# Kernel optimization log

Measured on AMD Instinct MI355X. Metric: run time of the kernel, lower is better.

Reference implementation:

```python
import jax, jax.numpy as jnp
import numpy as np

NUM_TOKENS = 16384
HIDDEN = 4096
NUM_EXPERTS = 256
TOP_K = 8
N_GROUP = 8
TOPK_GROUP = 4
NORM_TOPK_PROB = True
ROUTED_SCALING_FACTOR = 1.0


def setup_inputs() -> dict:
    key = jax.random.key(0)
    k1, k2, k3 = jax.random.split(key, 3)
    hidden_states = jax.random.normal(k1, (NUM_TOKENS, HIDDEN), dtype=jnp.float32)
    weight = jax.random.normal(k2, (NUM_EXPERTS, HIDDEN), dtype=jnp.float32) * (HIDDEN ** -0.5)
    e_score_correction_bias = jax.random.normal(k3, (NUM_EXPERTS,), dtype=jnp.float32) * 0.01
    return {"hidden_states": hidden_states, "weight": weight,
            "e_score_correction_bias": e_score_correction_bias}


def reference(hidden_states, weight, e_score_correction_bias):
    num_tokens = hidden_states.shape[0]
    # router logits: [T, E]
    logits = jnp.einsum('th,eh->te', hidden_states.astype(jnp.float32),
                        weight.astype(jnp.float32))
    scores = jax.nn.sigmoid(logits)
    scores_for_choice = scores + e_score_correction_bias[None, :]
    # group scores: sum of top-2 within each group, [T, G]
    per_group = scores_for_choice.reshape(num_tokens, N_GROUP, NUM_EXPERTS // N_GROUP)
    top2_vals, _ = jax.lax.top_k(per_group, 2)
    group_scores = top2_vals.sum(axis=-1)
    # select topk_group groups, build mask over experts
    _, group_idx = jax.lax.top_k(group_scores, TOPK_GROUP)  # [T, topk_group]
    group_mask = jnp.zeros_like(group_scores).at[
        jnp.arange(num_tokens)[:, None], group_idx].set(1.0)  # [T, G]
    score_mask = jnp.repeat(group_mask, NUM_EXPERTS // N_GROUP, axis=1)  # [T, E]
    tmp_scores = jnp.where(score_mask > 0, scores_for_choice, -jnp.inf)
    # final top-k experts over masked scores
    _, topk_idx = jax.lax.top_k(tmp_scores, TOP_K)  # [T, K]
    topk_weight = jnp.take_along_axis(scores, topk_idx, axis=1)
    if TOP_K > 1 and NORM_TOPK_PROB:
        denom = topk_weight.sum(axis=-1, keepdims=True) + 1e-20
        topk_weight = topk_weight / denom
    topk_weight = topk_weight * ROUTED_SCALING_FACTOR
    return logits, topk_weight, topk_idx
```

## Files before the change

kernel.cpp:

```cpp
#include <hip/hip_runtime.h>
#include <hip/hip_bf16.h>
#include <math.h>

#define TKN 16384
#define HID 4096
#define NE  256
#define TOPK 8
#define NGRP 8
#define TOPG 4

#define BM 64
#define BK 64
#define NKT (HID / BK)
#define BIMG 16384

typedef _Float16 half8 __attribute__((ext_vector_type(8)));
typedef float    f32x4 __attribute__((ext_vector_type(4)));

static __device__ __forceinline__ unsigned pkrtz(float x, float y) {
    auto r = __builtin_amdgcn_cvt_pkrtz(x, y);
    return __builtin_bit_cast(unsigned, r);
}
static __device__ __forceinline__ float hi_mask(float a) {
    return __uint_as_float(__float_as_uint(a) & 0xFFFFE000u);
}
static __device__ __forceinline__ void split_w(const float4 v,
    unsigned char* hiP, unsigned char* loP, int ofs)
{
    const float h0 = hi_mask(v.x), h1 = hi_mask(v.y),
                h2 = hi_mask(v.z), h3 = hi_mask(v.w);
    *(uint2*)(hiP + ofs) = make_uint2(pkrtz(h0, h1), pkrtz(h2, h3));
    *(uint2*)(loP + ofs) = make_uint2(pkrtz(v.x - h0, v.y - h1),
                                      pkrtz(v.z - h2, v.w - h3));
}

__global__ __launch_bounds__(256) void prep_b(const float* __restrict__ B,
                                              unsigned char* __restrict__ ws)
{
    const int gid = blockIdx.x * 256 + threadIdx.x;
    const int e   = gid >> 9;
    const int k0  = (gid & 511) * 8;
    const float* src = B + (size_t)e * HID + k0;
    float v[8];
    #pragma unroll
    for (int i = 0; i < 8; ++i) v[i] = src[i];
    unsigned hw[4], lw[4];
    #pragma unroll
    for (int j = 0; j < 4; ++j) {
        const float x0 = v[2*j], x1 = v[2*j+1];
        const float h0 = hi_mask(x0), h1 = hi_mask(x1);
        hw[j] = pkrtz(h0, h1);
        lw[j] = pkrtz(x0 - h0, x1 - h1);
    }
    const int cb     = e >> 6;
    const int colgrp = (e & 63) >> 4;
    const int lane16 = e & 15;
    const int kt     = k0 >> 6;
    const int kk     = k0 & 63;
    const int wg     = kk >> 5;
    const int kseg   = (kk >> 3) & 3;
    const int f      = colgrp * 2 + wg;
    unsigned char* img = ws + (size_t)(cb * NKT + kt) * BIMG
                            + f * 2048 + (kseg * 16 + lane16) * 16;
    *(uint4*)(img)        = make_uint4(hw[0], hw[1], hw[2], hw[3]);
    *(uint4*)(img + 1024) = make_uint4(lw[0], lw[1], lw[2], lw[3]);
}

__global__ __launch_bounds__(256, 3) void gemm_mfma(
    const float* __restrict__ A, const unsigned char* __restrict__ Bws,
    float* __restrict__ C)
{
    __shared__ __align__(16) unsigned char smem[2][2][8192];

    const int tid  = threadIdx.x;
    const int lane = tid & 63;
    const int wave = tid >> 6;
    const int wg = wave >> 1;
    const int wc = wave & 1;

    const int logical = (blockIdx.x & 7) * 128 + (blockIdx.x >> 3);
    const int mb   = logical >> 2;
    const int cb   = logical & 3;
    const int row0 = mb * BM;

    const float* srcp[4];
    int wofs[4];
    #pragma unroll
    for (int i = 0; i < 4; ++i) {
        const int r = i * 16 + wave * 4 + (lane >> 4);
        srcp[i] = A + (size_t)(row0 + r) * HID + (lane & 15) * 4;
        wofs[i] = r * 128 + (((lane & 15) * 8) ^ ((r & 7) << 4));
    }

    const int kx    = ((wg * 64) + ((lane >> 4) << 4)) ^ ((lane & 7) << 4);
    const int aRowB = (lane & 15) * 128;

    const unsigned char* bBase = Bws + (size_t)cb * NKT * BIMG;
    const int f0off = ((wc * 2 + 0) * 2 + wg) * 2048 + lane * 16;
    const int f1off = ((wc * 2 + 1) * 2 + wg) * 2048 + lane * 16;

    f32x4 acc[4][2];
    #pragma unroll
    for (int i = 0; i < 4; ++i) { acc[i][0] = (f32x4)0.f; acc[i][1] = (f32x4)0.f; }

    float4 aA[4], aB[4];
    half8  bA[4], bB[4];

    {
        float4 p[4];
        #pragma unroll
        for (int i = 0; i < 4; ++i) p[i] = *(const float4*)(srcp[i]);
        #pragma unroll
        for (int i = 0; i < 4; ++i)
            split_w(p[i], &smem[0][0][0], &smem[0][1][0], wofs[i]);
    }
    #pragma unroll
    for (int i = 0; i < 4; ++i) aB[i] = *(const float4*)(srcp[i] + BK);
    bA[0] = *(const half8*)(bBase + f0off);
    bA[1] = *(const half8*)(bBase + f0off + 1024);
    bA[2] = *(const half8*)(bBase + f1off);
    bA[3] = *(const half8*)(bBase + f1off + 1024);
    __syncthreads();

#define PSTEP(T, RBUF, WBUF, ASPL, AISS, BCUR, BNXT)                           \
    {                                                                          \
        const int t_ = (T);                                                    \
        if (t_ + 2 < NKT) {               \
            _Pragma("unroll")                                                  \
            for (int i = 0; i < 4; ++i)                                        \
                AISS[i] = *(const float4*)(srcp[i] + (t_ + 2) * BK);           \
        }                                                                      \
        if (t_ + 1 < NKT) {               \
            const unsigned char* bp = bBase + (size_t)(t_ + 1) * BIMG;         \
            BNXT[0] = *(const half8*)(bp + f0off);                             \
            BNXT[1] = *(const half8*)(bp + f0off + 1024);                      \
            BNXT[2] = *(const half8*)(bp + f1off);                             \
            BNXT[3] = *(const half8*)(bp + f1off + 1024);                      \
        }                                                                      \
                     \
        asm volatile("s_waitcnt lgkmcnt(0)\n\ts_barrier" ::: "memory");        \
        if (t_ + 1 < NKT) {         \
            _Pragma("unroll")                                                  \
            for (int i = 0; i < 4; ++i)                                        \
                split_w(ASPL[i], &WBUF[0][0], &WBUF[1][0], wofs[i]);           \
        }                                                                      \
        _Pragma("unroll")                                                      \
        for (int mt = 0; mt < 4; ++mt) {                                       \
            const half8 ah = *(const half8*)(&RBUF[0][0] + aRowB + mt * 2048 + kx); \
            const half8 al = *(const half8*)(&RBUF[1][0] + aRowB + mt * 2048 + kx); \
            f32x4 c0 = acc[mt][0];                                             \
            c0 = __builtin_amdgcn_mfma_f32_16x16x32_f16(ah, BCUR[0], c0, 0, 0, 0); \
            c0 = __builtin_amdgcn_mfma_f32_16x16x32_f16(ah, BCUR[1], c0, 0, 0, 0); \
            c0 = __builtin_amdgcn_mfma_f32_16x16x32_f16(al, BCUR[0], c0, 0, 0, 0); \
            acc[mt][0] = c0;                                                   \
            f32x4 c1 = acc[mt][1];                                             \
            c1 = __builtin_amdgcn_mfma_f32_16x16x32_f16(ah, BCUR[2], c1, 0, 0, 0); \
            c1 = __builtin_amdgcn_mfma_f32_16x16x32_f16(ah, BCUR[3], c1, 0, 0, 0); \
            c1 = __builtin_amdgcn_mfma_f32_16x16x32_f16(al, BCUR[3 - 1], c1, 0, 0, 0); \
            acc[mt][1] = c1;                                                   \
        }                                                                      \
    }

    for (int kt = 0; kt < NKT; kt += 2) {
        PSTEP(kt,     smem[0], smem[1], aB, aA, bA, bB);
        PSTEP(kt + 1, smem[1], smem[0], aA, aB, bB, bA);
    }
#undef PSTEP

    float* redf = (float*)&smem[0][0][0];
    const int fb = wc * 2048 + lane * 4;
    if (wg == 1) {
        #pragma unroll
        for (int mt = 0; mt < 4; ++mt)
            #pragma unroll
            for (int nt = 0; nt < 2; ++nt)
                *(f32x4*)&redf[fb + (mt * 2 + nt) * 256] = acc[mt][nt];
    }
    __syncthreads();
    if (wg == 0) {
        #pragma unroll
        for (int mt = 0; mt < 4; ++mt) {
            #pragma unroll
            for (int nt = 0; nt < 2; ++nt) {
                f32x4 o = acc[mt][nt] + *(const f32x4*)&redf[fb + (mt * 2 + nt) * 256];
                const int r0 = row0 + mt * 16 + (lane >> 4) * 4;
                const int cc = cb * 64 + wc * 32 + nt * 16 + (lane & 15);
                #pragma unroll
                for (int r = 0; r < 4; ++r)
                    C[(size_t)(r0 + r) * NE + cc] = o[r];
            }
        }
    }
}

__global__ __launch_bounds__(256) void router_topk_kernel(
    const float* __restrict__ logits, const float* __restrict__ bias,
    float* __restrict__ out_w, float* __restrict__ out_i)
{
    const int wid  = threadIdx.x >> 6;
    const int lane = threadIdx.x & 63;
    const int token = blockIdx.x * 4 + wid;

    const float* row = logits + (size_t)token * NE;
    const float4 lg = *(const float4*)&row[lane * 4];

    float sig[4], sc[4];
    {
        const float l4[4] = {lg.x, lg.y, lg.z, lg.w};
        #pragma unroll
        for (int j = 0; j < 4; ++j) {
            sig[j] = 1.f / (1.f + expf(-l4[j]));
            sc[j]  = sig[j] + bias[lane * 4 + j];
        }
    }

    float m1 = sc[0], m2 = -INFINITY;
    #pragma unroll
    for (int j = 1; j < 4; ++j) {
        if (sc[j] > m1) { m2 = m1; m1 = sc[j]; }
        else if (sc[j] > m2) { m2 = sc[j]; }
    }
    #pragma unroll
    for (int off = 1; off < 8; off <<= 1) {
        const float o1 = __shfl_xor(m1, off);
        const float o2 = __shfl_xor(m2, off);
        const float lo = fminf(m1, o1);
        m1 = fmaxf(m1, o1);
        m2 = fmaxf(lo, fmaxf(m2, o2));
    }
    const float gscore = m1 + m2;

    const int gmy = lane >> 3;
    int rank = 0;
    #pragma unroll
    for (int g = 0; g < NGRP; ++g) {
        const float gs = __shfl(gscore, g * 8);
        if (gs > gscore || (gs == gscore && g < gmy)) ++rank;
    }
    if (rank >= TOPG) {
        #pragma unroll
        for (int j = 0; j < 4; ++j) sc[j] = -INFINITY;
    }

    float wk[TOPK]; int ik[TOPK];
    float wsum = 0.f;
    #pragma unroll
    for (int k = 0; k < TOPK; ++k) {
        float bv = sc[0]; int bi = lane * 4;
        #pragma unroll
        for (int j = 1; j < 4; ++j)
            if (sc[j] > bv) { bv = sc[j]; bi = lane * 4 + j; }
        #pragma unroll
        for (int off = 1; off < 64; off <<= 1) {
            const float v2 = __shfl_xor(bv, off);
            const int   i2 = __shfl_xor(bi, off);
            if (v2 > bv || (v2 == bv && i2 < bi)) { bv = v2; bi = i2; }
        }
        const int owner = bi >> 2;
        const int j = bi & 3;
        const float sv = (j == 0) ? sig[0] : (j == 1) ? sig[1] : (j == 2) ? sig[2] : sig[3];
        const float w = __shfl(sv, owner);
        wk[k] = w; ik[k] = bi; wsum += w;
        if (lane == owner) {
            if (j == 0) sc[0] = -INFINITY;
            else if (j == 1) sc[1] = -INFINITY;
            else if (j == 2) sc[2] = -INFINITY;
            else sc[3] = -INFINITY;
        }
    }

    if (lane == 0) {
        const float denom = wsum + 1e-20f;
        #pragma unroll
        for (int k = 0; k < TOPK; ++k) {
            out_w[(size_t)token * TOPK + k] = wk[k] / denom;
            out_i[(size_t)token * TOPK + k] = (float)ik[k];
        }
    }
}

extern "C" void kernel_launch(void* const* d_in, const int* in_sizes, int n_in,
                              void* d_out, int out_size, void* d_ws, size_t ws_size,
                              hipStream_t stream) {
    const float* hidden = (const float*)d_in[0];
    const float* weight = (const float*)d_in[1];
    const float* bias   = (const float*)d_in[2];

    float* logits = (float*)d_out;
    float* out_w  = logits + (size_t)TKN * NE;
    float* out_i  = out_w + (size_t)TKN * TOPK;

    unsigned char* bpl = (unsigned char*)d_ws;

    prep_b<<<512, 256, 0, stream>>>(weight, bpl);
    gemm_mfma<<<1024, 256, 0, stream>>>(hidden, bpl, logits);
    router_topk_kernel<<<TKN / 4, 256, 0, stream>>>(logits, bias, out_w, out_i);
}
```

Measured before the change: 169.9 us.

## Deepen A-tile register prefetch to three stages and hoist LDS fragment reads

Rotates four register buffers for the fp32 A tile so global loads are issued three k-steps ahead instead of two. The loop is unrolled by four, with sched_barriers pinning load issue order. All A fragments for the current tile are read from LDS before the split-and-write of the next tile, so the LDS reads overlap the conversion work and the MFMAs see ready operands. This costs more VGPRs, which may lower occupancy.

```diff
diff --git a/kernel.cpp b/kernel.cpp
--- a/kernel.cpp
+++ b/kernel.cpp
@@ -103,67 +103,81 @@
     #pragma unroll
     for (int i = 0; i < 4; ++i) { acc[i][0] = (f32x4)0.f; acc[i][1] = (f32x4)0.f; }
 
-    float4 aA[4], aB[4];
+    float4 a0[4], a1[4], a2[4], a3[4];
     half8  bA[4], bB[4];
 
-    {
-        float4 p[4];
-        #pragma unroll
-        for (int i = 0; i < 4; ++i) p[i] = *(const float4*)(srcp[i]);
-        #pragma unroll
-        for (int i = 0; i < 4; ++i)
-            split_w(p[i], &smem[0][0][0], &smem[0][1][0], wofs[i]);
-    }
-    #pragma unroll
-    for (int i = 0; i < 4; ++i) aB[i] = *(const float4*)(srcp[i] + BK);
+    #pragma unroll
+    for (int i = 0; i < 4; ++i) a0[i] = *(const float4*)(srcp[i]);
+    #pragma unroll
+    for (int i = 0; i < 4; ++i) a1[i] = *(const float4*)(srcp[i] + BK);
+    #pragma unroll
+    for (int i = 0; i < 4; ++i) a2[i] = *(const float4*)(srcp[i] + 2 * BK);
     bA[0] = *(const half8*)(bBase + f0off);
     bA[1] = *(const half8*)(bBase + f0off + 1024);
     bA[2] = *(const half8*)(bBase + f1off);
     bA[3] = *(const half8*)(bBase + f1off + 1024);
+    #pragma unroll
+    for (int i = 0; i < 4; ++i)
+        split_w(a0[i], &smem[0][0][0], &smem[0][1][0], wofs[i]);
     __syncthreads();
 
-#define PSTEP(T, RBUF, WBUF, ASPL, AISS, BCUR, BNXT)                           \
+#define PSTEP(T, ASPL, AISS, BCUR, BNXT)                                       \
     {                                                                          \
         const int t_ = (T);                                                    \
-        if (t_ + 2 < NKT) {               \
-            _Pragma("unroll")                                                  \
-            for (int i = 0; i < 4; ++i)                                        \
-                AISS[i] = *(const float4*)(srcp[i] + (t_ + 2) * BK);           \
-        }                                                                      \
-        if (t_ + 1 < NKT) {               \
+        if (t_ + 1 < NKT) {                    \
             const unsigned char* bp = bBase + (size_t)(t_ + 1) * BIMG;         \
             BNXT[0] = *(const half8*)(bp + f0off);                             \
             BNXT[1] = *(const half8*)(bp + f0off + 1024);                      \
             BNXT[2] = *(const half8*)(bp + f1off);                             \
             BNXT[3] = *(const half8*)(bp + f1off + 1024);                      \
         }                                                                      \
-                     \
-        asm volatile("s_waitcnt lgkmcnt(0)\n\ts_barrier" ::: "memory");        \
-        if (t_ + 1 < NKT) {         \
+        __builtin_amdgcn_sched_barrier(0);                                     \
+        if (t_ + 3 < NKT) {                 \
             _Pragma("unroll")                                                  \
             for (int i = 0; i < 4; ++i)                                        \
-                split_w(ASPL[i], &WBUF[0][0], &WBUF[1][0], wofs[i]);           \
-        }                                                                      \
+                AISS[i] = *(const float4*)(srcp[i] + (t_ + 3) * BK);           \
+        }                                                                      \
+        __builtin_amdgcn_sched_barrier(0);                                     \
+                  \
+        asm volatile("s_waitcnt lgkmcnt(0)\n\ts_barrier" ::: "memory");        \
+                          \
+        half8 ah[4], al[4];                                                    \
+        {                                                                      \
+            const unsigned char* rb = &smem[t_ & 1][0][0];                     \
+            _Pragma("unroll")                                                  \
+            for (int mt = 0; mt < 4; ++mt) {                                   \
+                ah[mt] = *(const half8*)(rb + aRowB + mt * 2048 + kx);         \
+                al[mt] = *(const half8*)(rb + 8192 + aRowB + mt * 2048 + kx);  \
+            }                                                                  \
+        }                                                                      \
+                    \
+        if (t_ + 1 < NKT) {                                                    \
+            unsigned char* wb = &smem[(t_ + 1) & 1][0][0];                     \
+            _Pragma("unroll")                                                  \
+            for (int i = 0; i < 4; ++i)                                        \
+                split_w(ASPL[i], wb, wb + 8192, wofs[i]);                      \
+        }                                                                      \
+                            \
         _Pragma("unroll")                                                      \
         for (int mt = 0; mt < 4; ++mt) {                                       \
-            const half8 ah = *(const half8*)(&RBUF[0][0] + aRowB + mt * 2048 + kx); \
-            const half8 al = *(const half8*)(&RBUF[1][0] + aRowB + mt * 2048 + kx); \
             f32x4 c0 = acc[mt][0];                                             \
-            c0 = __builtin_amdgcn_mfma_f32_16x16x32_f16(ah, BCUR[0], c0, 0, 0, 0); \
-            c0 = __builtin_amdgcn_mfma_f32_16x16x32_f16(ah, BCUR[1], c0, 0, 0, 0); \
-            c0 = __builtin_amdgcn_mfma_f32_16x16x32_f16(al, BCUR[0], c0, 0, 0, 0); \
+            c0 = __builtin_amdgcn_mfma_f32_16x16x32_f16(ah[mt], BCUR[0], c0, 0, 0, 0); \
+            c0 = __builtin_amdgcn_mfma_f32_16x16x32_f16(ah[mt], BCUR[1], c0, 0, 0, 0); \
+            c0 = __builtin_amdgcn_mfma_f32_16x16x32_f16(al[mt], BCUR[0], c0, 0, 0, 0); \
             acc[mt][0] = c0;                                                   \
             f32x4 c1 = acc[mt][1];                                             \
-            c1 = __builtin_amdgcn_mfma_f32_16x16x32_f16(ah, BCUR[2], c1, 0, 0, 0); \
-            c1 = __builtin_amdgcn_mfma_f32_16x16x32_f16(ah, BCUR[3], c1, 0, 0, 0); \
-            c1 = __builtin_amdgcn_mfma_f32_16x16x32_f16(al, BCUR[3 - 1], c1, 0, 0, 0); \
+            c1 = __builtin_amdgcn_mfma_f32_16x16x32_f16(ah[mt], BCUR[2], c1, 0, 0, 0); \
+            c1 = __builtin_amdgcn_mfma_f32_16x16x32_f16(ah[mt], BCUR[3], c1, 0, 0, 0); \
+            c1 = __builtin_amdgcn_mfma_f32_16x16x32_f16(al[mt], BCUR[2], c1, 0, 0, 0); \
             acc[mt][1] = c1;                                                   \
         }                                                                      \
     }
 
-    for (int kt = 0; kt < NKT; kt += 2) {
-        PSTEP(kt,     smem[0], smem[1], aB, aA, bA, bB);
-        PSTEP(kt + 1, smem[1], smem[0], aA, aB, bB, bA);
+    for (int kt = 0; kt < NKT; kt += 4) {
+        PSTEP(kt + 0, a1, a3, bA, bB);
+        PSTEP(kt + 1, a2, a0, bB, bA);
+        PSTEP(kt + 2, a3, a1, bA, bB);
+        PSTEP(kt + 3, a0, a2, bB, bA);
     }
 #undef PSTEP
 
```

Result: slower. 395.2 us (+132.6%).
